# Kernel optimization log

Measured on AMD Instinct MI355X. Metric: run time of the kernel, lower is better.

Reference implementation:

```python
import jax, jax.numpy as jnp
import numpy as np

B, L, D, K = 32, 200, 768, 8  # batch, seq_len, bert dim, max_span_length
S = int(sum(L - 1 - k for k in range(1, K + 1)))  # 1556 total spans for a full sentence


def setup_inputs() -> dict:
    key = jax.random.key(0)
    ks = jax.random.split(key, 20)
    features = jax.random.normal(ks[0], (B, L, D), dtype=jnp.float32)
    lengths = jax.random.randint(ks[1], (B,), K + 4, L + 1)  # valid token counts incl CLS/SEP
    mask = (jnp.arange(L)[None, :] < lengths[:, None]).astype(jnp.int32)
    span_mask = jnp.ones((B, S), dtype=jnp.int32)
    inp = {"features": features, "mask": mask, "span_mask": span_mask}
    for j in range(K - 1):
        k = j + 2
        inp[f"w{k}"] = jax.random.normal(ks[2 + j], (D, D, k), dtype=jnp.float32) * 0.02
        inp[f"b{k}"] = jax.random.normal(ks[10 + j], (D,), dtype=jnp.float32) * 0.02
    return inp


def _feature_slice(features, mask, num_spans, ws, bs):
    # features: [B, L, D]; mask: [B, L] (ones then zeros); ws[j]: Conv1d weight [D, D, j+2]
    Bb, Ll, Dd = features.shape
    Kk = len(ws) + 1  # max_span_length
    x = features.transpose(0, 2, 1)  # [B, D, L] (NCH)
    sources = [features]  # k=0: unigram features
    for w, b in zip(ws, bs):
        y = jax.lax.conv_general_dilated(x, w, (1,), "VALID", dimension_numbers=("NCH", "OIH", "NCH"))
        y = (y + b[None, :, None]).transpose(0, 2, 1)  # [B, L-k+1, D]
        sources.append(jnp.pad(y, ((0, 0), (0, Ll - y.shape[1]), (0, 0))))
    src = jnp.stack(sources, 0)  # [K, B, L, D]
    n = jnp.sum(mask, axis=1)  # valid lengths incl CLS/SEP
    # span-length k+1 contributes max(n - k - 2, 0) spans, sources start at index 1
    counts = jnp.maximum(n[:, None] - jnp.arange(Kk)[None, :] - 2, 0)  # [B, K]
    offsets = jnp.concatenate([jnp.zeros((Bb, 1), counts.dtype), jnp.cumsum(counts, axis=1)], axis=1)  # [B, K+1]
    s = jnp.arange(num_spans)
    kidx = jnp.sum(offsets[:, 1:Kk, None] <= s[None, None, :], axis=1)  # [B, S] bucket per slot
    pos = jnp.clip(s[None, :] - jnp.take_along_axis(offsets, kidx, axis=1) + 1, 0, Ll - 1)  # [B, S]
    valid = s[None, :] < offsets[:, Kk:Kk + 1]  # [B, S]
    out = src[kidx, jnp.arange(Bb)[:, None], pos] * valid[:, :, None].astype(features.dtype)
    return out, valid.astype(jnp.int32)


def reference(features, mask, span_mask, w2, w3, w4, w5, w6, w7, w8, b2, b3, b4, b5, b6, b7, b8):
    ws = (w2, w3, w4, w5, w6, w7, w8)
    bs = (b2, b3, b4, b5, b6, b7, b8)
    return _feature_slice(features, mask, span_mask.shape[1], ws, bs)
```

## Files before the change

### kernel.cpp

```cpp
#include <hip/hip_runtime.h>
#include <hip/hip_bf16.h>

#define BB 32
#define LL 200
#define DD 768
#define SS 1556
#define MAXM 6400

typedef __attribute__((ext_vector_type(8))) short bf16x8;
typedef __attribute__((ext_vector_type(4))) float floatx4;

__device__ __forceinline__ float bf2f(ushort u){
    union { unsigned int i; float f; } v; v.i = ((unsigned int)u) << 16; return v.f;
}
__device__ __forceinline__ ushort f2bf(float f){
    union { float f; unsigned int i; } v; v.f = f;
    unsigned int x = v.i;
    return (ushort)((x + 0x7FFFu + ((x >> 16) & 1u)) >> 16);
}

__device__ const int GCNT_C[8] = {5,5,5,5,5,5,6,6};
__device__ const int GLIST_C[8][6] = {
    {36,37,38, 0, 4, 0},
    {39,40,41, 1, 5, 0},
    {30,31,32, 6, 2, 0},
    {33,34,35, 7, 3, 0},
    {24,25,26,12,13, 0},
    {27,28,29,14,15, 0},
    {18,19,20,16, 8,10},
    {21,22,23,17, 9,11},
};

__global__ void detect_kernel(const unsigned int* __restrict__ feat_raw, int* __restrict__ flag){
    __shared__ int cnt_s;
    if (threadIdx.x == 0) cnt_s = 0;
    __syncthreads();
    int c = 0;
    for (int i = threadIdx.x; i < 4096; i += 256){
        unsigned int w = feat_raw[i];
        unsigned int e = (w >> 7) & 0xFFu;
        if (e >= 100u && e <= 150u) c++;
    }
    atomicAdd(&cnt_s, c);
    __syncthreads();
    if (threadIdx.x == 0) *flag = (cnt_s > 2457) ? 1 : 0;
}

__global__ void offs_kernel(const int* __restrict__ mask, int* __restrict__ offs){
    int b = blockIdx.x;
    int lane = threadIdx.x;
    int s = 0;
    for (int i = lane; i < LL; i += 64) s += mask[b*LL + i];
    #pragma unroll
    for (int d = 32; d > 0; d >>= 1) s += __shfl_down(s, d, 64);
    if (lane == 0){
        int n = s, cum = 0;
        offs[b*9 + 0] = 0;
        for (int j = 0; j < 8; ++j){
            int c = n - j - 2; if (c < 0) c = 0;
            cum += c;
            offs[b*9 + j + 1] = cum;
        }
    }
}

__global__ void maps_kernel(const int* __restrict__ offs, int* __restrict__ pfx,
                            int* __restrict__ amap, int* __restrict__ omap){
    const int kkidx = blockIdx.x;
    const int kk = kkidx + 2;
    __shared__ int P[33];
    __shared__ int base_s[32];
    const int tid = threadIdx.x;
    if (tid == 0){
        int acc = 0; P[0] = 0;
        for (int b = 0; b < 32; ++b){
            acc += offs[b*9 + kk] - offs[b*9 + kk - 1];
            P[b+1] = acc;
        }
    }
    if (tid < 32) base_s[tid] = offs[tid*9 + kk - 1];
    __syncthreads();
    if (tid == 0) pfx[kkidx*33 + 32] = P[32];
    const int Mtot = P[32];
    for (int r = tid; r < MAXM; r += 256){
        int b = 0;
        #pragma unroll
        for (int i = 1; i <= 32; ++i) b += (P[i] <= r) ? 1 : 0;
        int bb = b < 32 ? b : 31;
        int larow = (r < Mtot) ? (r - P[bb]) : 0;
        amap[kkidx*MAXM + r] = bb*LL + larow + 1;
        omap[kkidx*MAXM + r] = bb*SS + base_s[bb] + larow;
    }
}

__global__ void repack2_kernel(const void* __restrict__ w2, const void* __restrict__ w3,
                               const void* __restrict__ w4, const void* __restrict__ w5,
                               const void* __restrict__ w6, const void* __restrict__ w7,
                               const void* __restrict__ w8,
                               const void* __restrict__ b2, const void* __restrict__ b3,
                               const void* __restrict__ b4, const void* __restrict__ b5,
                               const void* __restrict__ b6, const void* __restrict__ b7,
                               const void* __restrict__ b8,
                               ushort* __restrict__ BpAll, float* __restrict__ biasF,
                               const int* __restrict__ flag){
    const int kkidx = blockIdx.y;
    const int kk = kkidx + 2;
    const void* w  = kkidx==0?w2:kkidx==1?w3:kkidx==2?w4:kkidx==3?w5:kkidx==4?w6:kkidx==5?w7:w8;
    const void* bv = kkidx==0?b2:kkidx==1?b3:kkidx==2?b4:kkidx==3?b5:kkidx==4?b6:kkidx==5?b7:b8;
    ushort* Bp = BpAll + (size_t)(kkidx*(kkidx+3)/2)*589824;

    const int bfm = *flag;
    __shared__ ushort lds[24576];
    const int tid = threadIdx.x;
    const int ob  = blockIdx.x;
    const int rowlen = DD * kk;
    const int nelem  = 4 * rowlen;

    if (bfm){
        const ushort* src = (const ushort*)w + (size_t)ob * nelem;
        const int nch = nelem >> 3;
        for (int c = tid; c < nch; c += 256)
            __builtin_memcpy(lds + c*8, src + c*8, 16);
        if (ob == 0)
            for (int i = tid; i < DD; i += 256) biasF[kkidx*DD + i] = bf2f(((const ushort*)bv)[i]);
    } else {
        const float* src = (const float*)w + (size_t)ob * nelem;
        const int nch = nelem >> 2;
        for (int c = tid; c < nch; c += 256){
            float t4[4];
            __builtin_memcpy(t4, src + c*4, 16);
            #pragma unroll
            for (int j2 = 0; j2 < 4; ++j2) lds[c*4 + j2] = f2bf(t4[j2]);
        }
        if (ob == 0)
            for (int i = tid; i < DD; i += 256) biasF[kkidx*DD + i] = ((const float*)bv)[i];
    }
    __syncthreads();

    const int total = 96 * kk * 4;
    for (int c = tid; c < total; c += 256){
        int jb = c >> 2, ol = c & 3;
        int j0 = jb * 8;
        int t  = j0 / 768;
        int i0 = j0 - t * 768;
        ushort tmp[8];
        #pragma unroll
        for (int jj = 0; jj < 8; ++jj)
            tmp[jj] = lds[ol*rowlen + (i0 + jj)*kk + t];
        int o = ob*4 + ol;
        __builtin_memcpy(Bp + (size_t)jb*6144 + (size_t)o*8, tmp, 16);
    }
}

__global__ void cvtA_kernel(const void* __restrict__ feat, ushort* __restrict__ featbf,
                            const int* __restrict__ flag){
    const int bfm = *flag;
    int idx = blockIdx.x*256 + threadIdx.x;
    const int TOT = BB*LL*DD/8;
    if (idx >= TOT) return;
    if (bfm){
        __builtin_memcpy(featbf + (size_t)idx*8, (const ushort*)feat + (size_t)idx*8, 16);
    } else {
        float t8[8];
        __builtin_memcpy(t8,     (const float*)feat + (size_t)idx*8,     16);
        __builtin_memcpy(t8 + 4, (const float*)feat + (size_t)idx*8 + 4, 16);
        ushort o8[8];
        #pragma unroll
        for (int j = 0; j < 8; ++j) o8[j] = f2bf(t8[j]);
        __builtin_memcpy(featbf + (size_t)idx*8, o8, 16);
    }
}

__global__ void fill_kernel(const void* __restrict__ feat, const int* __restrict__ offs,
                            void* __restrict__ out, const int* __restrict__ flag){
    const int bfm = *flag;
    int idx = blockIdx.x*256 + threadIdx.x;
    const int TOT = BB*SS*192;
    if (idx >= TOT) return;
    int b = idx / (SS*192);
    int r = idx - b*(SS*192);
    int s = r / 192;
    int c = r - s*192;
    int c0  = offs[b*9 + 1];
    int tot = offs[b*9 + 8];
    if (bfm){
        if (c < 96){
            ushort* dst = (ushort*)out + ((size_t)b*SS + s)*768 + c*8;
            if (s < c0){
                const ushort* srcp = (const ushort*)feat + ((size_t)b*LL + s + 1)*768 + c*8;
                __builtin_memcpy(dst, srcp, 16);
            } else if (s >= tot){
                const ushort z[8] = {0,0,0,0,0,0,0,0};
                __builtin_memcpy(dst, z, 16);
            }
        }
        if (c == 0)
            ((ushort*)out)[(size_t)BB*SS*768 + (size_t)b*SS + s] = (s < tot) ? (ushort)0x3F80 : (ushort)0;
    } else {
        float* dst = (float*)out + ((size_t)b*SS + s)*768 + c*4;
        if (s < c0){
            const float* srcp = (const float*)feat + ((size_t)b*LL + s + 1)*768 + c*4;
            __builtin_memcpy(dst, srcp, 16);
        } else if (s >= tot){
            const float z[4] = {0.f,0.f,0.f,0.f};
            __builtin_memcpy(dst, z, 16);
        }
        if (c == 0)
            ((float*)out)[(size_t)BB*SS*768 + (size_t)b*SS + s] = (s < tot) ? 1.0f : 0.0f;
    }
}

__global__ __launch_bounds__(256) void conv_gemm5(const ushort* __restrict__ featbf,
        const ushort* __restrict__ BpAll, const float* __restrict__ biasF,
        const int* __restrict__ pfx, const int* __restrict__ amap,
        const int* __restrict__ omap, void* __restrict__ out,
        const int* __restrict__ flag){
    const int n   = blockIdx.x;
    const int xcd = n & 7;
    const int is  = n >> 3;
    const int cx  = GCNT_C[xcd];
    if (is >= cx * 50) return;
    int p = is / 100;
    int r = is - p*100;
    int gi, mt;
    if (2*p + 1 < cx){ gi = 2*p + (r & 1); mt = r >> 1; }
    else             { gi = 2*p;           mt = r;      }
    const int g  = GLIST_C[xcd][gi];
    const int kkidx = g / 6;
    const int nt = g - kkidx*6;
    const int kk = kkidx + 2;
    const int Mtot = pfx[kkidx*33 + 32];
    const int m0 = mt * 128;
    if (m0 >= Mtot) return;
    const int n0 = nt * 128;
    const int bfm = *flag;

    __shared__ ushort BsA[2][8192];
    __shared__ ushort BsB[2][8192];

    const int tid  = threadIdx.x;
    const int wv   = tid >> 6;
    const int wvm  = wv >> 1;
    const int wvn  = wv & 1;
    const int lane = tid & 63;
    const int quad = lane >> 4;
    const int l15  = lane & 15;
    const int wvbase = tid & 192;

    const ushort* srcA[4];
    #pragma unroll
    for (int j = 0; j < 4; ++j){
        int g2 = j*4 + wv;
        int wvm_s = g2 >> 3, sm_s = (g2 >> 1) & 3, ks_s = g2 & 1;
        int rr = kkidx*MAXM + m0 + wvm_s*64 + sm_s*16 + l15;
        srcA[j] = featbf + (size_t)amap[rr]*768 + ks_s*32 + quad*8;
    }

    floatx4 acc[4][4];
    #pragma unroll
    for (int sn = 0; sn < 4; ++sn){
        float bv = biasF[kkidx*768 + n0 + wvn*64 + sn*16 + l15];
        #pragma unroll
        for (int sm = 0; sm < 4; ++sm){
            acc[sm][sn][0] = bv; acc[sm][sn][1] = bv;
            acc[sm][sn][2] = bv; acc[sm][sn][3] = bv;
        }
    }

    const ushort* BkkBase = BpAll + (size_t)(kkidx*(kkidx+3)/2)*589824;
    const ushort* bsrc0 = BkkBase + (size_t)(tid >> 7)*6144 + (size_t)(n0 + (tid & 127))*8;
    char* ldsA = (char*)&BsA[0][0];
    char* ldsB = (char*)&BsB[0][0];
    const int nchunks = kk * 12;

    #define STAGE_A(ABUF, ch) do { \
        _Pragma("unroll") \
        for (int j_ = 0; j_ < 4; ++j_){ \
            __builtin_amdgcn_global_load_lds( \
                (const __attribute__((address_space(1))) void*)(srcA[j_] + (ch)*64), \
                (__attribute__((address_space(3))) void*)(ldsA + (ABUF)*16384 + (j_*256 + wvbase)*16), \
                16, 0, 0); \
        } } while(0)

    #define STAGE_B(BBUF, ch) do { \
        const ushort* gb_ = bsrc0 + (size_t)(ch)*8*6144; \
        _Pragma("unroll") \
        for (int ii_ = 0; ii_ < 4; ++ii_){ \
            __builtin_amdgcn_global_load_lds( \
                (const __attribute__((address_space(1))) void*)(gb_ + (size_t)ii_*2*6144), \
                (__attribute__((address_space(3))) void*)(ldsB + (BBUF)*16384 + (ii_*256 + wvbase)*16), \
                16, 0, 0); \
        } } while(0)

    #define COMPUTE(ABUF, BBUF) do { \
        __builtin_amdgcn_s_setprio(1); \
        _Pragma("unroll") \
        for (int ks_ = 0; ks_ < 2; ++ks_){ \
            const int pl_ = ks_*4 + quad; \
            bf16x8 afr[4], bfr[4]; \
            _Pragma("unroll") \
            for (int sm_ = 0; sm_ < 4; ++sm_) \
                __builtin_memcpy(&afr[sm_], \
                    ldsA + (ABUF)*16384 + (wvm*8 + sm_*2 + ks_)*1024 + lane*16, 16); \
            _Pragma("unroll") \
            for (int sn_ = 0; sn_ < 4; ++sn_) \
                __builtin_memcpy(&bfr[sn_], &BsB[BBUF][pl_*1024 + (wvn*64 + sn_*16 + l15)*8], 16); \
            _Pragma("unroll") \
            for (int sm_ = 0; sm_ < 4; ++sm_) \
                _Pragma("unroll") \
                for (int sn_ = 0; sn_ < 4; ++sn_) \
                    acc[sm_][sn_] = __builtin_amdgcn_mfma_f32_16x16x32_bf16( \
                        afr[sm_], bfr[sn_], acc[sm_][sn_], 0, 0, 0); \
        } \
        __builtin_amdgcn_s_setprio(0); \
        } while(0)

    #define SUBSTEP(CH, CUR, NXT, DO, NW) do { \
        if (DO){ STAGE_A(NXT, (CH)+1); STAGE_B(NXT, (CH)+1); } \
        __builtin_amdgcn_sched_barrier(0); \
        asm volatile("s_waitcnt vmcnt(" NW ")" ::: "memory"); \
        __builtin_amdgcn_sched_barrier(0); \
        __builtin_amdgcn_s_barrier(); \
        __builtin_amdgcn_sched_barrier(0); \
        COMPUTE(CUR, CUR); \
        __builtin_amdgcn_s_barrier(); \
        __builtin_amdgcn_sched_barrier(0); \
    } while(0)

    STAGE_A(0, 0);
    STAGE_B(0, 0);

    for (int ch = 0; ch < nchunks - 2; ch += 2){
        SUBSTEP(ch,   0, 1, true, "8");
        SUBSTEP(ch+1, 1, 0, true, "8");
    }
    SUBSTEP(nchunks-2, 0, 1, true,  "8");
    SUBSTEP(nchunks-1, 1, 0, false, "0");

    #undef SUBSTEP
    #undef STAGE_A
    #undef STAGE_B
    #undef COMPUTE

    #pragma unroll
    for (int sm = 0; sm < 4; ++sm){
        #pragma unroll
        for (int rr = 0; rr < 4; ++rr){
            int r2 = m0 + wvm*64 + sm*16 + quad*4 + rr;
            if (r2 < Mtot){
                int slot = omap[kkidx*MAXM + r2];
                if (bfm){
                    ushort* oh = (ushort*)out;
                    #pragma unroll
                    for (int sn = 0; sn < 4; ++sn)
                        oh[(size_t)slot*768 + n0 + wvn*64 + sn*16 + l15] = f2bf(acc[sm][sn][rr]);
                } else {
                    float* of = (float*)out;
                    #pragma unroll
                    for (int sn = 0; sn < 4; ++sn)
                        of[(size_t)slot*768 + n0 + wvn*64 + sn*16 + l15] = acc[sm][sn][rr];
                }
            }
        }
    }
}

__global__ __launch_bounds__(256) void conv_gemm_direct(const void* __restrict__ feat,
        const int* __restrict__ offs, void* __restrict__ out, const int* __restrict__ flag,
        const void* w2, const void* w3, const void* w4, const void* w5,
        const void* w6, const void* w7, const void* w8,
        const void* b2, const void* b3, const void* b4, const void* b5,
        const void* b6, const void* b7, const void* b8){
    const int bfm = *flag;
    const int kkidx = blockIdx.y;
    const int kk = kkidx + 2;
    const int b = blockIdx.z;
    const void* w  = kkidx==0?w2:kkidx==1?w3:kkidx==2?w4:kkidx==3?w5:kkidx==4?w6:kkidx==5?w7:w8;
    const void* bv = kkidx==0?b2:kkidx==1?b3:kkidx==2?b4:kkidx==3?b5:kkidx==4?b6:kkidx==5?b7:b8;

    const int off_j = offs[b*9 + kk - 1];
    const int cnt   = offs[b*9 + kk] - off_j;
    const int mt = blockIdx.x / 12;
    const int nt = blockIdx.x - mt*12;
    const int m0 = mt * 64;
    if (m0 >= cnt) return;
    const int n0 = nt * 64;

    const int tid  = threadIdx.x;
    const int wvv  = tid >> 6;
    const int lane = tid & 63;
    const int quad = lane >> 4;
    const int l15  = lane & 15;

    int row  = m0 + wvv*16 + l15;
    int arow = row < cnt ? row : cnt - 1;
    const size_t abase = ((size_t)b*LL + arow + 1)*768 + quad*8;

    floatx4 acc[4];
    #pragma unroll
    for (int cg = 0; cg < 4; ++cg){
        float bb = bfm ? bf2f(((const ushort*)bv)[n0 + cg*16 + l15])
                       : ((const float*)bv)[n0 + cg*16 + l15];
        acc[cg][0] = bb; acc[cg][1] = bb; acc[cg][2] = bb; acc[cg][3] = bb;
    }

    const int steps = kk * 24;
    for (int s = 0; s < steps; ++s){
        bf16x8 a;
        if (bfm){
            __builtin_memcpy(&a, (const ushort*)feat + abase + s*32, 16);
        } else {
            float t8[8];
            __builtin_memcpy(t8,     (const float*)feat + abase + s*32,     16);
            __builtin_memcpy(t8 + 4, (const float*)feat + abase + s*32 + 4, 16);
            ushort o8[8];
            #pragma unroll
            for (int j = 0; j < 8; ++j) o8[j] = f2bf(t8[j]);
            __builtin_memcpy(&a, o8, 16);
        }
        int j0 = s*32 + quad*8;
        int t  = j0 / 768;
        int i0 = j0 - t*768;
        #pragma unroll
        for (int cg = 0; cg < 4; ++cg){
            int o = n0 + cg*16 + l15;
            size_t wbase = (size_t)o*(DD*kk) + (size_t)i0*kk + t;
            ushort tmp[8];
            if (bfm){
                const ushort* wp = (const ushort*)w + wbase;
                #pragma unroll
                for (int jj = 0; jj < 8; ++jj) tmp[jj] = wp[(size_t)jj*kk];
            } else {
                const float* wp = (const float*)w + wbase;
                #pragma unroll
                for (int jj = 0; jj < 8; ++jj) tmp[jj] = f2bf(wp[(size_t)jj*kk]);
            }
            bf16x8 bfr;
            __builtin_memcpy(&bfr, tmp, 16);
            acc[cg] = __builtin_amdgcn_mfma_f32_16x16x32_bf16(a, bfr, acc[cg], 0, 0, 0);
        }
    }

    const int rbase = m0 + wvv*16 + quad*4;
    if (bfm){
        ushort* outh = (ushort*)out;
        #pragma unroll
        for (int cg = 0; cg < 4; ++cg)
            #pragma unroll
            for (int rr = 0; rr < 4; ++rr){
                int grow = rbase + rr;
                if (grow < cnt)
                    outh[((size_t)b*SS + off_j + grow)*768 + n0 + cg*16 + l15] = f2bf(acc[cg][rr]);
            }
    } else {
        float* outf = (float*)out;
        #pragma unroll
        for (int cg = 0; cg < 4; ++cg)
            #pragma unroll
            for (int rr = 0; rr < 4; ++rr){
                int grow = rbase + rr;
                if (grow < cnt)
                    outf[((size_t)b*SS + off_j + grow)*768 + n0 + cg*16 + l15] = acc[cg][rr];
            }
    }
}

extern "C" void kernel_launch(void* const* d_in, const int* in_sizes, int n_in,
                              void* d_out, int out_size, void* d_ws, size_t ws_size,
                              hipStream_t stream) {
    const void* feat = d_in[0];
    const int*  mask = (const int*)d_in[1];

    const void* w[7]  = {0,0,0,0,0,0,0};
    const void* bs[7] = {0,0,0,0,0,0,0};
    int bi = 0;
    for (int i = 3; i < n_in; ++i){
        if (in_sizes[i] == 768){
            if (bi < 7) bs[bi++] = d_in[i];
        } else {
            int kk = in_sizes[i] / 589824;
            if (kk >= 2 && kk <= 8) w[kk-2] = d_in[i];
        }
    }

    char* ws = (char*)d_ws;
    int*    flag    = (int*)ws;
    int*    offs    = (int*)(ws + 64);
    int*    pfx     = (int*)(ws + 2048);
    float*  biasF   = (float*)(ws + 4096);
    int*    amap    = (int*)(ws + 28672);
    int*    omap    = (int*)(ws + 28672 + 179200);
    ushort* featbf  = (ushort*)(ws + 393216);
    ushort* Bp      = (ushort*)(ws + 393216 + 9830400);
    const size_t FULL_BYTES = 393216ull + 9830400ull + 41287680ull;
    const bool use_full = ws_size >= FULL_BYTES;

    hipLaunchKernelGGL(detect_kernel, dim3(1), dim3(256), 0, stream,
                       (const unsigned int*)feat, flag);
    hipLaunchKernelGGL(offs_kernel, dim3(BB), dim3(64), 0, stream, mask, offs);

    if (use_full){
        hipLaunchKernelGGL(repack2_kernel, dim3(192, 7), dim3(256), 0, stream,
                           w[0], w[1], w[2], w[3], w[4], w[5], w[6],
                           bs[0], bs[1], bs[2], bs[3], bs[4], bs[5], bs[6],
                           Bp, biasF, flag);
        hipLaunchKernelGGL(cvtA_kernel, dim3(2400), dim3(256), 0, stream, feat, featbf, flag);
        hipLaunchKernelGGL(maps_kernel, dim3(7), dim3(256), 0, stream, offs, pfx, amap, omap);
    }

    hipLaunchKernelGGL(fill_kernel, dim3((BB*SS*192 + 255)/256), dim3(256), 0, stream,
                       feat, offs, d_out, flag);

    if (use_full){
        hipLaunchKernelGGL(conv_gemm5, dim3(2400), dim3(256), 0, stream,
                           featbf, Bp, biasF, pfx, amap, omap, d_out, flag);
    } else {
        hipLaunchKernelGGL(conv_gemm_direct, dim3(48, 7, BB), dim3(256), 0, stream,
                           feat, offs, d_out, flag,
                           w[0], w[1], w[2], w[3], w[4], w[5], w[6],
                           bs[0], bs[1], bs[2], bs[3], bs[4], bs[5], bs[6]);
    }
}
```

Before: 562.7 us.

## Enlarge conv GEMM tiles to 256x256 with 512-thread blocks and rework XCD scheduling

The conv GEMM kernel moves from 128x128 tiles with 256 threads to 256x256 tiles with 512 threads. It uses a single unified LDS buffer and a K-chunk of 32, and each wave now computes a 4x8 grid of MFMA fragments. The group-to-XCD assignment table is rebuilt for the new tile counts, and the fill kernel is remapped to one block per (span, batch). The larger tiles raise data reuse per LDS load and cut the number of blocks. The cost is higher register pressure (launch_bounds 512,2), more synchronisation steps, and coarser M-tile padding waste.

Measured after the change: 563.9 us. Within noise of the previous version (+0.2%).

```diff
diff --git a/kernel.cpp b/kernel.cpp
--- a/kernel.cpp
+++ b/kernel.cpp
@@ -19,16 +19,16 @@
     return (ushort)((x + 0x7FFFu + ((x >> 16) & 1u)) >> 16);
 }
 
-__device__ const int GCNT_C[8] = {5,5,5,5,5,5,6,6};
-__device__ const int GLIST_C[8][6] = {
-    {36,37,38, 0, 4, 0},
-    {39,40,41, 1, 5, 0},
-    {30,31,32, 6, 2, 0},
-    {33,34,35, 7, 3, 0},
-    {24,25,26,12,13, 0},
-    {27,28,29,14,15, 0},
-    {18,19,20,16, 8,10},
-    {21,22,23,17, 9,11},
+__device__ const int GCNT2[8] = {2,2,2,2,2,2,4,5};
+__device__ const int GLIST2[8][5] = {
+    {18, 9, 0, 0, 0},
+    {19,10, 0, 0, 0},
+    {20,11, 0, 0, 0},
+    {15,12, 0, 0, 0},
+    {16,13, 0, 0, 0},
+    {17,14, 0, 0, 0},
+    { 6, 7, 3, 0, 0},
+    { 8, 4, 5, 1, 2},
 };
 
 __global__ void detect_kernel(const unsigned int* __restrict__ feat_raw, int* __restrict__ flag){
@@ -171,46 +171,44 @@
     }
 }
 
-__global__ void fill_kernel(const void* __restrict__ feat, const int* __restrict__ offs,
-                            void* __restrict__ out, const int* __restrict__ flag){
+__global__ void fill2_kernel(const void* __restrict__ feat, const int* __restrict__ offs,
+                             void* __restrict__ out, const int* __restrict__ flag){
+    const int s = blockIdx.x;
+    const int b = blockIdx.y;
     const int bfm = *flag;
-    int idx = blockIdx.x*256 + threadIdx.x;
-    const int TOT = BB*SS*192;
-    if (idx >= TOT) return;
-    int b = idx / (SS*192);
-    int r = idx - b*(SS*192);
-    int s = r / 192;
-    int c = r - s*192;
-    int c0  = offs[b*9 + 1];
-    int tot = offs[b*9 + 8];
+    const int tid = threadIdx.x;
+    const int c0  = offs[b*9 + 1];
+    const int tot = offs[b*9 + 8];
     if (bfm){
-        if (c < 96){
-            ushort* dst = (ushort*)out + ((size_t)b*SS + s)*768 + c*8;
+        if (tid < 96){
+            ushort* dst = (ushort*)out + ((size_t)b*SS + s)*768 + tid*8;
             if (s < c0){
-                const ushort* srcp = (const ushort*)feat + ((size_t)b*LL + s + 1)*768 + c*8;
+                const ushort* srcp = (const ushort*)feat + ((size_t)b*LL + s + 1)*768 + tid*8;
                 __builtin_memcpy(dst, srcp, 16);
             } else if (s >= tot){
                 const ushort z[8] = {0,0,0,0,0,0,0,0};
                 __builtin_memcpy(dst, z, 16);
             }
-        }
-        if (c == 0)
+        } else if (tid == 96){
             ((ushort*)out)[(size_t)BB*SS*768 + (size_t)b*SS + s] = (s < tot) ? (ushort)0x3F80 : (ushort)0;
+        }
     } else {
-        float* dst = (float*)out + ((size_t)b*SS + s)*768 + c*4;
-        if (s < c0){
-            const float* srcp = (const float*)feat + ((size_t)b*LL + s + 1)*768 + c*4;
-            __builtin_memcpy(dst, srcp, 16);
-        } else if (s >= tot){
-            const float z[4] = {0.f,0.f,0.f,0.f};
-            __builtin_memcpy(dst, z, 16);
-        }
-        if (c == 0)
+        if (tid < 192){
+            float* dst = (float*)out + ((size_t)b*SS + s)*768 + tid*4;
+            if (s < c0){
+                const float* srcp = (const float*)feat + ((size_t)b*LL + s + 1)*768 + tid*4;
+                __builtin_memcpy(dst, srcp, 16);
+            } else if (s >= tot){
+                const float z[4] = {0.f,0.f,0.f,0.f};
+                __builtin_memcpy(dst, z, 16);
+            }
+        } else if (tid == 192){
             ((float*)out)[(size_t)BB*SS*768 + (size_t)b*SS + s] = (s < tot) ? 1.0f : 0.0f;
-    }
-}
-
-__global__ __launch_bounds__(256) void conv_gemm5(const ushort* __restrict__ featbf,
+        }
+    }
+}
+
+__global__ __launch_bounds__(512, 2) void conv_gemm7(const ushort* __restrict__ featbf,
         const ushort* __restrict__ BpAll, const float* __restrict__ biasF,
         const int* __restrict__ pfx, const int* __restrict__ amap,
         const int* __restrict__ omap, void* __restrict__ out,
@@ -218,25 +216,21 @@
     const int n   = blockIdx.x;
     const int xcd = n & 7;
     const int is  = n >> 3;
-    const int cx  = GCNT_C[xcd];
-    if (is >= cx * 50) return;
-    int p = is / 100;
-    int r = is - p*100;
-    int gi, mt;
-    if (2*p + 1 < cx){ gi = 2*p + (r & 1); mt = r >> 1; }
-    else             { gi = 2*p;           mt = r;      }
-    const int g  = GLIST_C[xcd][gi];
-    const int kkidx = g / 6;
-    const int nt = g - kkidx*6;
+    const int cx  = GCNT2[xcd];
+    if (is >= cx * 25) return;
+    const int gi = is % cx;
+    const int mt = is / cx;
+    const int g  = GLIST2[xcd][gi];
+    const int kkidx = g / 3;
+    const int nt = g - kkidx*3;
     const int kk = kkidx + 2;
     const int Mtot = pfx[kkidx*33 + 32];
-    const int m0 = mt * 128;
+    const int m0 = mt * 256;
     if (m0 >= Mtot) return;
-    const int n0 = nt * 128;
+    const int n0 = nt * 256;
     const int bfm = *flag;
 
-    __shared__ ushort BsA[2][8192];
-    __shared__ ushort BsB[2][8192];
+    __shared__ ushort LDSbuf[32768];
 
     const int tid  = threadIdx.x;
     const int wv   = tid >> 6;
@@ -245,21 +239,26 @@
     const int lane = tid & 63;
     const int quad = lane >> 4;
     const int l15  = lane & 15;
-    const int wvbase = tid & 192;
-
-    const ushort* srcA[4];
+
+    const ushort* srcA[2];
     #pragma unroll
-    for (int j = 0; j < 4; ++j){
-        int g2 = j*4 + wv;
-        int wvm_s = g2 >> 3, sm_s = (g2 >> 1) & 3, ks_s = g2 & 1;
-        int rr = kkidx*MAXM + m0 + wvm_s*64 + sm_s*16 + l15;
-        srcA[j] = featbf + (size_t)amap[rr]*768 + ks_s*32 + quad*8;
-    }
-
-    floatx4 acc[4][4];
+    for (int j = 0; j < 2; ++j){
+        int g2 = j*8 + wv;
+        int rr = kkidx*MAXM + m0 + (g2 >> 2)*64 + (g2 & 3)*16 + l15;
+        srcA[j] = featbf + (size_t)amap[rr]*768 + quad*8;
+    }
+    const ushort* BkkBase = BpAll + (size_t)(kkidx*(kkidx+3)/2)*589824;
+    const ushort* srcB[2];
     #pragma unroll
-    for (int sn = 0; sn < 4; ++sn){
-        float bv = biasF[kkidx*768 + n0 + wvn*64 + sn*16 + l15];
+    for (int j = 0; j < 2; ++j){
+        int c = j*512 + tid;
+        srcB[j] = BkkBase + (size_t)(c >> 8)*6144 + (size_t)(n0 + (c & 255))*8;
+    }
+
+    floatx4 acc[4][8];
+    #pragma unroll
+    for (int sn = 0; sn < 8; ++sn){
+        float bv = biasF[kkidx*768 + n0 + wvn*128 + sn*16 + l15];
         #pragma unroll
         for (int sm = 0; sm < 4; ++sm){
             acc[sm][sn][0] = bv; acc[sm][sn][1] = bv;
@@ -267,79 +266,64 @@
         }
     }
 
-    const ushort* BkkBase = BpAll + (size_t)(kkidx*(kkidx+3)/2)*589824;
-    const ushort* bsrc0 = BkkBase + (size_t)(tid >> 7)*6144 + (size_t)(n0 + (tid & 127))*8;
-    char* ldsA = (char*)&BsA[0][0];
-    char* ldsB = (char*)&BsB[0][0];
-    const int nchunks = kk * 12;
-
-    #define STAGE_A(ABUF, ch) do { \
+    char* lds0 = (char*)&LDSbuf[0];
+    const int nchunks = kk * 24;
+
+    #define STAGE(BUF, ch) do { \
         _Pragma("unroll") \
-        for (int j_ = 0; j_ < 4; ++j_){ \
+        for (int j_ = 0; j_ < 2; ++j_) \
             __builtin_amdgcn_global_load_lds( \
-                (const __attribute__((address_space(1))) void*)(srcA[j_] + (ch)*64), \
-                (__attribute__((address_space(3))) void*)(ldsA + (ABUF)*16384 + (j_*256 + wvbase)*16), \
+                (const __attribute__((address_space(1))) void*)(srcA[j_] + (ch)*32), \
+                (__attribute__((address_space(3))) void*)(lds0 + (BUF)*32768 + (j_*512 + tid)*16), \
                 16, 0, 0); \
-        } } while(0)
-
-    #define STAGE_B(BBUF, ch) do { \
-        const ushort* gb_ = bsrc0 + (size_t)(ch)*8*6144; \
         _Pragma("unroll") \
-        for (int ii_ = 0; ii_ < 4; ++ii_){ \
+        for (int j_ = 0; j_ < 2; ++j_) \
             __builtin_amdgcn_global_load_lds( \
-                (const __attribute__((address_space(1))) void*)(gb_ + (size_t)ii_*2*6144), \
-                (__attribute__((address_space(3))) void*)(ldsB + (BBUF)*16384 + (ii_*256 + wvbase)*16), \
+                (const __attribute__((address_space(1))) void*)(srcB[j_] + (size_t)(ch)*24576), \
+                (__attribute__((address_space(3))) void*)(lds0 + (BUF)*32768 + 16384 + (j_*512 + tid)*16), \
                 16, 0, 0); \
-        } } while(0)
-
-    #define COMPUTE(ABUF, BBUF) do { \
+        } while(0)
+
+    #define COMPUTE(BUF) do { \
+        bf16x8 afr[4], bfr[8]; \
+        _Pragma("unroll") \
+        for (int sm_ = 0; sm_ < 4; ++sm_) \
+            __builtin_memcpy(&afr[sm_], lds0 + (BUF)*32768 + (wvm*4 + sm_)*1024 + lane*16, 16); \
+        _Pragma("unroll") \
+        for (int sn_ = 0; sn_ < 8; ++sn_) \
+            __builtin_memcpy(&bfr[sn_], lds0 + (BUF)*32768 + 16384 + quad*4096 + (wvn*128 + sn_*16 + l15)*16, 16); \
         __builtin_amdgcn_s_setprio(1); \
         _Pragma("unroll") \
-        for (int ks_ = 0; ks_ < 2; ++ks_){ \
-            const int pl_ = ks_*4 + quad; \
-            bf16x8 afr[4], bfr[4]; \
+        for (int sm_ = 0; sm_ < 4; ++sm_) \
             _Pragma("unroll") \
-            for (int sm_ = 0; sm_ < 4; ++sm_) \
-                __builtin_memcpy(&afr[sm_], \
-                    ldsA + (ABUF)*16384 + (wvm*8 + sm_*2 + ks_)*1024 + lane*16, 16); \
-            _Pragma("unroll") \
-            for (int sn_ = 0; sn_ < 4; ++sn_) \
-                __builtin_memcpy(&bfr[sn_], &BsB[BBUF][pl_*1024 + (wvn*64 + sn_*16 + l15)*8], 16); \
-            _Pragma("unroll") \
-            for (int sm_ = 0; sm_ < 4; ++sm_) \
-                _Pragma("unroll") \
-                for (int sn_ = 0; sn_ < 4; ++sn_) \
-                    acc[sm_][sn_] = __builtin_amdgcn_mfma_f32_16x16x32_bf16( \
-                        afr[sm_], bfr[sn_], acc[sm_][sn_], 0, 0, 0); \
-        } \
+            for (int sn_ = 0; sn_ < 8; ++sn_) \
+                acc[sm_][sn_] = __builtin_amdgcn_mfma_f32_16x16x32_bf16( \
+                    afr[sm_], bfr[sn_], acc[sm_][sn_], 0, 0, 0); \
         __builtin_amdgcn_s_setprio(0); \
         } while(0)
 
     #define SUBSTEP(CH, CUR, NXT, DO, NW) do { \
-        if (DO){ STAGE_A(NXT, (CH)+1); STAGE_B(NXT, (CH)+1); } \
+        if (DO) STAGE(NXT, (CH)+1); \
         __builtin_amdgcn_sched_barrier(0); \
         asm volatile("s_waitcnt vmcnt(" NW ")" ::: "memory"); \
         __builtin_amdgcn_sched_barrier(0); \
         __builtin_amdgcn_s_barrier(); \
         __builtin_amdgcn_sched_barrier(0); \
-        COMPUTE(CUR, CUR); \
+        COMPUTE(CUR); \
         __builtin_amdgcn_s_barrier(); \
         __builtin_amdgcn_sched_barrier(0); \
     } while(0)
 
-    STAGE_A(0, 0);
-    STAGE_B(0, 0);
-
+    STAGE(0, 0);
     for (int ch = 0; ch < nchunks - 2; ch += 2){
-        SUBSTEP(ch,   0, 1, true, "8");
-        SUBSTEP(ch+1, 1, 0, true, "8");
-    }
-    SUBSTEP(nchunks-2, 0, 1, true,  "8");
+        SUBSTEP(ch,   0, 1, true, "4");
+        SUBSTEP(ch+1, 1, 0, true, "4");
+    }
+    SUBSTEP(nchunks-2, 0, 1, true,  "4");
     SUBSTEP(nchunks-1, 1, 0, false, "0");
 
     #undef SUBSTEP
-    #undef STAGE_A
-    #undef STAGE_B
+    #undef STAGE
     #undef COMPUTE
 
     #pragma unroll
@@ -352,13 +336,13 @@
                 if (bfm){
                     ushort* oh = (ushort*)out;
                     #pragma unroll
-                    for (int sn = 0; sn < 4; ++sn)
-                        oh[(size_t)slot*768 + n0 + wvn*64 + sn*16 + l15] = f2bf(acc[sm][sn][rr]);
+                    for (int sn = 0; sn < 8; ++sn)
+                        oh[(size_t)slot*768 + n0 + wvn*128 + sn*16 + l15] = f2bf(acc[sm][sn][rr]);
                 } else {
                     float* of = (float*)out;
                     #pragma unroll
-                    for (int sn = 0; sn < 4; ++sn)
-                        of[(size_t)slot*768 + n0 + wvn*64 + sn*16 + l15] = acc[sm][sn][rr];
+                    for (int sn = 0; sn < 8; ++sn)
+                        of[(size_t)slot*768 + n0 + wvn*128 + sn*16 + l15] = acc[sm][sn][rr];
                 }
             }
         }
@@ -508,11 +492,11 @@
         hipLaunchKernelGGL(maps_kernel, dim3(7), dim3(256), 0, stream, offs, pfx, amap, omap);
     }
 
-    hipLaunchKernelGGL(fill_kernel, dim3((BB*SS*192 + 255)/256), dim3(256), 0, stream,
+    hipLaunchKernelGGL(fill2_kernel, dim3(SS, BB), dim3(256), 0, stream,
                        feat, offs, d_out, flag);
 
     if (use_full){
-        hipLaunchKernelGGL(conv_gemm5, dim3(2400), dim3(256), 0, stream,
+        hipLaunchKernelGGL(conv_gemm7, dim3(1000), dim3(512), 0, stream,
                            featbf, Bp, biasF, pfx, amap, omap, d_out, flag);
     } else {
         hipLaunchKernelGGL(conv_gemm_direct, dim3(48, 7, BB), dim3(256), 0, stream,
```
